# Kernel optimization log

Measured on AMD Instinct MI355X. Metric: run time of the kernel, lower is better.

Reference implementation:

```python
import jax, jax.numpy as jnp
import numpy as np

EMB_DIM = 128
MID = 192  # ceil(1.5 * emb_dim)
VOCAB = 3000
KCLS = 5
B = 16
S = 128
EPS = 1e-5


def _linear_init(k, fin, fout):
    k1, k2 = jax.random.split(k)
    bound = 1.0 / np.sqrt(fin)
    W = jax.random.uniform(k1, (fin, fout), minval=-bound, maxval=bound, dtype=jnp.float32)
    b = jax.random.uniform(k2, (fout,), minval=-bound, maxval=bound, dtype=jnp.float32)
    return W, b


def setup_inputs() -> dict:
    key = jax.random.key(0)
    ks = jax.random.split(key, 7)
    emb = jax.random.normal(ks[0], (VOCAB, EMB_DIM), dtype=jnp.float32)
    W1, b1 = _linear_init(ks[1], 2 * EMB_DIM, MID)   # encoder layer 1
    W2, b2 = _linear_init(ks[2], MID, EMB_DIM)       # encoder layer 2
    W3, b3 = _linear_init(ks[3], EMB_DIM, MID)       # decoder layer 1
    W4, b4 = _linear_init(ks[4], MID, 2 * EMB_DIM)   # decoder layer 2
    Wk, bk = _linear_init(ks[5], EMB_DIM, KCLS)      # soft head
    inputs = jax.random.randint(ks[6], (B, S), 0, VOCAB, dtype=jnp.int64)
    return dict(inputs=inputs, emb=emb, W1=W1, b1=b1, W2=W2, b2=b2,
                W3=W3, b3=b3, W4=W4, b4=b4, Wk=Wk, bk=bk)


def _forward(inputs, emb, W1, b1, W2, b2, W3, b3, W4, b4, Wk, bk):
    X = emb[inputs]                      # (B,S,m)
    Bs, Sl, m = X.shape
    bidx = jnp.arange(Bs)
    karr = jnp.arange(Sl)
    jarr = jnp.arange(Sl - 1)

    def step(carry, t):
        nodes, counts, acc = carry       # (B,S,m), (B,S), (B,)
        L = Sl - t                       # current active list length
        right, left = nodes[:, 1:], nodes[:, :-1]          # pair j = (node[j+1], node[j])
        y = (jnp.concatenate([right, left], -1) @ W1 + b1) @ W2 + b2   # (B,S-1,m)
        xx = (y @ W3 + b3) @ W4 + b4                                    # (B,S-1,2m)
        # torch cross_entropy with float-vector target: -sum(target * log_softmax(input))
        ls1 = -(right * jax.nn.log_softmax(xx[..., :m], -1)).sum(-1)
        ls2 = -(left * jax.nn.log_softmax(xx[..., m:], -1)).sum(-1)
        n1, n2 = counts[:, 1:], counts[:, :-1]
        loss = ((n1 + EPS) * ls1 + (n2 + EPS) * ls2) / (n1 + n2 + EPS)
        valid = jarr < (L - 1)                                          # only first L-1 pairs active
        idx = jnp.argmin(jnp.where(valid[None, :], loss, jnp.inf), axis=1)  # (B,)
        acc = acc + jnp.take_along_axis(loss, idx[:, None], 1)[:, 0]
        father_x = jnp.take_along_axis(y, idx[:, None, None], 1)[:, 0]  # (B,m)
        # faithful bug: lc = nodelist[idx-1] (python wrap to L-1 when idx==0), rc = nodelist[idx]
        lc_idx = jnp.where(idx == 0, L - 1, idx - 1)
        father_cnt = (jnp.take_along_axis(counts, idx[:, None], 1)[:, 0]
                      + jnp.take_along_axis(counts, lc_idx[:, None], 1)[:, 0])
        pos = jnp.maximum(idx - 1, 0)
        # new list: drop lc and rc, father lands at pos; gather map reproduces list insert/remove
        src = jnp.where((idx[:, None] == 0) | (karr[None, :] < idx[:, None] - 1),
                        karr[None, :], karr[None, :] + 1)
        src = jnp.minimum(src, Sl - 1)
        nodes = jnp.take_along_axis(nodes, src[:, :, None], 1).at[bidx, pos].set(father_x)
        counts = jnp.take_along_axis(counts, src, 1).at[bidx, pos].set(father_cnt)
        return (nodes, counts, acc), None

    init = (X, jnp.ones((Bs, Sl), X.dtype), jnp.zeros((Bs,), X.dtype))
    (nodes, counts, acc), _ = jax.lax.scan(step, init, jnp.arange(Sl - 1))
    pred = jnp.argmax(nodes[:, 0] @ Wk + bk, axis=-1)   # argmax softmax == argmax logits
    return pred, acc.sum() / Bs


def reference(inputs, emb, W1, b1, W2, b2, W3, b3, W4, b4, Wk, bk):
    return _forward(inputs, emb, W1, b1, W2, b2, W3, b3, W4, b4, Wk, bk)
```

## Files before the change

kernel.cpp:

```cpp
#include <hip/hip_runtime.h>
#include <math.h>

#define EMB 128
#define MID 192
#define SEQ 128
#define BATCH 16
#define NPAIR 127
#define KCLS 5
#define EPSF 1e-5f

#define OFF_WYT   0
#define OFF_BY    32768
#define OFF_WXXT  32896
#define OFF_BXX   65664
#define OFF_NODES 65920
#define OFF_YC    328064
#define OFF_L0    588160

__global__ void k_comp(const float* __restrict__ W1, const float* __restrict__ b1,
                       const float* __restrict__ W2, const float* __restrict__ b2,
                       const float* __restrict__ W3, const float* __restrict__ b3,
                       const float* __restrict__ W4, const float* __restrict__ b4,
                       float* __restrict__ ws) {
    int tid = blockIdx.x * blockDim.x + threadIdx.x;
    if (tid < 32768) {
        int k = tid >> 7, o = tid & 127;
        float a = 0.f;
        for (int j = 0; j < MID; ++j) a += W1[k*MID+j] * W2[j*EMB+o];
        int ch = k >> 5, jj = k & 31;
        ws[OFF_WYT + (size_t)(o*8 + ch)*32 + jj] = a;
    } else if (tid < 65536) {
        int t = tid - 32768;
        int k = t >> 8, c = t & 255;
        float a = 0.f;
        for (int j = 0; j < MID; ++j) a += W3[k*MID+j] * W4[j*256+c];
        int ch = k >> 5, jj = k & 31;
        ws[OFF_WXXT + (size_t)(c*4 + ch)*32 + jj] = a;
    } else if (tid < 65536 + 128) {
        int o = tid - 65536;
        float a = b2[o];
        for (int j = 0; j < MID; ++j) a += b1[j] * W2[j*EMB+o];
        ws[OFF_BY + o] = a;
    } else if (tid < 65536 + 128 + 256) {
        int o = tid - 65536 - 128;
        float a = b4[o];
        for (int j = 0; j < MID; ++j) a += b3[j] * W4[j*256+o];
        ws[OFF_BXX + o] = a;
    }
}

__global__ void k_nodes(const int* __restrict__ inp, const float* __restrict__ emb,
                        float* __restrict__ ws) {
    int tid = blockIdx.x * blockDim.x + threadIdx.x;
    if (tid >= BATCH*SEQ*EMB) return;
    int d = tid & 127;
    int bs = tid >> 7;
    int tok = inp[bs];
    ws[OFF_NODES + tid] = emb[tok*EMB + d];
}

#define DPPF(x, ctrl) __int_as_float(__builtin_amdgcn_update_dpp(0, __float_as_int(x), (ctrl), 0xF, 0xF, true))
#define DPPI(x, ctrl) __builtin_amdgcn_update_dpp(0, (x), (ctrl), 0xF, 0xF, true)
#define SWZ4F(x)  __int_as_float(__builtin_amdgcn_ds_swizzle(__float_as_int(x), 0x101F))
#define SWZ16F(x) __int_as_float(__builtin_amdgcn_ds_swizzle(__float_as_int(x), 0x401F))
#define SWZ16I(x) __builtin_amdgcn_ds_swizzle((x), 0x401F)

__global__ void __launch_bounds__(512, 1) k_init(float* __restrict__ ws) {
    __shared__ float s_x[2][2*EMB];
    __shared__ float s_red[4][2][EMB];
    __shared__ float s_redx[2][2][256];
    __shared__ float s_y[2][EMB];
    __shared__ float s_by[EMB];
    __shared__ float s_bxx[2*EMB];
    __shared__ float s_ls[2][2];
    int tid = threadIdx.x;
    int b = blockIdx.x >> 3, g = blockIdx.x & 7;
    int q4 = tid >> 7, o = tid & 127;
    int hh = tid >> 8, c = tid & 255;
    float wy[64], wxx[64];
    {
        const float4* gw = (const float4*)(ws + OFF_WYT);
        #pragma unroll
        for (int i = 0; i < 16; ++i) {
            float4 v = gw[((size_t)o*8 + q4*2 + (i>>3))*8 + (i&7)];
            wy[4*i]=v.x; wy[4*i+1]=v.y; wy[4*i+2]=v.z; wy[4*i+3]=v.w;
        }
        const float4* gx = (const float4*)(ws + OFF_WXXT);
        #pragma unroll
        for (int i = 0; i < 16; ++i) {
            float4 v = gx[((size_t)c*4 + hh*2 + (i>>3))*8 + (i&7)];
            wxx[4*i]=v.x; wxx[4*i+1]=v.y; wxx[4*i+2]=v.z; wxx[4*i+3]=v.w;
        }
    }
    if (tid < EMB) s_by[tid] = ws[OFF_BY + tid];
    if (tid < 2*EMB) s_bxx[tid] = ws[OFF_BXX + tid];
    const float* nodes = ws + OFF_NODES + (size_t)b*SEQ*EMB;
    float* yc = ws + OFF_YC + (size_t)b*NPAIR*EMB;
    int p_s = tid >> 8, kk = tid & 255;
    __syncthreads();
    for (int i = 0; i < 8; ++i) {
        int base = g*16 + i*2;
        {
            int j = base + p_s;
            int jj = j < NPAIR ? j : NPAIR - 1;
            s_x[p_s][kk] = nodes[(jj + (kk < 128 ? 1 : 0))*EMB + (kk & 127)];
        }
        __syncthreads();
        float a0 = 0.f, a1 = 0.f;
        #pragma unroll
        for (int j = 0; j < 64; ++j) {
            float w = wy[j];
            a0 += s_x[0][q4*64 + j] * w;
            a1 += s_x[1][q4*64 + j] * w;
        }
        s_red[q4][0][o] = a0;
        s_red[q4][1][o] = a1;
        __syncthreads();
        if (tid < 256) {
            int p = tid >> 7, oo = tid & 127;
            float yv = s_red[0][p][oo] + s_red[1][p][oo] + s_red[2][p][oo] + s_red[3][p][oo] + s_by[oo];
            s_y[p][oo] = yv;
            int j2 = base + p;
            if (j2 < NPAIR) yc[(size_t)j2*EMB + oo] = yv;
        }
        __syncthreads();
        float c0 = 0.f, c1 = 0.f;
        #pragma unroll
        for (int j = 0; j < 64; ++j) {
            float w = wxx[j];
            c0 += s_y[0][hh*64 + j] * w;
            c1 += s_y[1][hh*64 + j] * w;
        }
        s_redx[hh][0][c] = c0;
        s_redx[hh][1][c] = c1;
        __syncthreads();
        if (tid < 256) {
            int w = tid >> 6, lane = tid & 63;
            int p2 = w >> 1, h2 = w & 1;
            int cA = h2*128 + lane, cB = cA + 64;
            float v0 = s_redx[0][p2][cA] + s_redx[1][p2][cA] + s_bxx[cA];
            float v1 = s_redx[0][p2][cB] + s_redx[1][p2][cB] + s_bxx[cB];
            float m = fmaxf(v0, v1);
            for (int s = 32; s; s >>= 1) m = fmaxf(m, __shfl_xor(m, s, 64));
            float se = expf(v0 - m) + expf(v1 - m);
            for (int s = 32; s; s >>= 1) se += __shfl_xor(se, s, 64);
            float lse = m + logf(se);
            float o0 = s_x[p2][cA], o1 = s_x[p2][cB];
            float term = o0*(v0 - lse) + o1*(v1 - lse);
            for (int s = 32; s; s >>= 1) term += __shfl_xor(term, s, 64);
            if (lane == 0) s_ls[p2][h2] = -term;
        }
        __syncthreads();
        if (tid < 2) {
            int j2 = base + tid;
            if (j2 < NPAIR) {
                float l = ((1.f+EPSF)*s_ls[tid][0] + (1.f+EPSF)*s_ls[tid][1]) / (2.f + EPSF);
                ws[OFF_L0 + b*NPAIR + j2] = l;
            }
        }
        __syncthreads();
    }
}

#define SX(p, c) s_x[p][(((c) >> 6)*72) + ((c) & 63)]

__global__ void __launch_bounds__(1024, 4) __attribute__((amdgpu_waves_per_eu(4, 4)))
k_seq(float* __restrict__ ws,
      const float* __restrict__ Wk, const float* __restrict__ bkv,
      float* __restrict__ out) {
    __shared__ float s_nodes[SEQ*EMB];
    __shared__ float s_yc[NPAIR*EMB];
    __shared__ float s_x[2][4*72];
    __shared__ float s_y[2][EMB];
    __shared__ float s_xx[2][2*EMB];
    __shared__ float s_by[EMB];
    __shared__ float s_bxx[2*EMB];
    __shared__ float s_ls[2][2];
    __shared__ float s_loss[2][SEQ];
    __shared__ float s_cnt[2][SEQ];
    __shared__ int   s_nslot[2][SEQ];
    __shared__ int   s_yslot[2][SEQ];
    __shared__ float s_restv[4];
    __shared__ int   s_resti[4];
    __shared__ float s_log[KCLS];

    int tid = threadIdx.x;
    int b = blockIdx.x;
    float wy32[32], wxx32[32];
    {
        const float4* gw = (const float4*)(ws + OFF_WYT) + (size_t)tid*8;
        #pragma unroll
        for (int i = 0; i < 8; ++i) { float4 v = gw[i]; wy32[4*i]=v.x; wy32[4*i+1]=v.y; wy32[4*i+2]=v.z; wy32[4*i+3]=v.w; }
        const float4* gx = (const float4*)(ws + OFF_WXXT) + (size_t)tid*8;
        #pragma unroll
        for (int i = 0; i < 8; ++i) { float4 v = gx[i]; wxx32[4*i]=v.x; wxx32[4*i+1]=v.y; wxx32[4*i+2]=v.z; wxx32[4*i+3]=v.w; }
    }
    {
        const float4* gn = (const float4*)(ws + OFF_NODES + (size_t)b*SEQ*EMB);
        float4* sn = (float4*)s_nodes;
        for (int i = tid; i < SEQ*EMB/4; i += 1024) sn[i] = gn[i];
        const float4* gy = (const float4*)(ws + OFF_YC + (size_t)b*NPAIR*EMB);
        float4* sy = (float4*)s_yc;
        for (int i = tid; i < NPAIR*EMB/4; i += 1024) sy[i] = gy[i];
    }
    if (tid < EMB) s_by[tid] = ws[OFF_BY + tid];
    if (tid < 2*EMB) s_bxx[tid] = ws[OFF_BXX + tid];
    if (tid < NPAIR) { s_loss[0][tid] = ws[OFF_L0 + b*NPAIR + tid]; s_yslot[0][tid] = tid; }
    if (tid < SEQ)   { s_cnt[0][tid] = 1.f; s_nslot[0][tid] = tid; }

    float acc = 0.f;
    int cur = 0;
    int q0c = -1, q1c = -1;
    const int ch1 = tid & 7,  o1 = tid >> 3;
    const int ch2 = tid & 3,  c2 = tid >> 2;
    const int sp = tid >> 8, skk = tid & 255;
    __syncthreads();

    #pragma unroll 1
    for (int t = 0; t < NPAIR; ++t) {
        const int L = SEQ - t;
        if (t > 0) {
            {
                float a0 = 0.f, a1 = 0.f;
                const float* x0 = &s_x[0][(ch1 >> 1)*72 + (ch1 & 1)*32];
                const float* x1 = &s_x[1][(ch1 >> 1)*72 + (ch1 & 1)*32];
                #pragma unroll
                for (int j = 0; j < 32; ++j) { float w = wy32[j]; a0 = fmaf(x0[j], w, a0); a1 = fmaf(x1[j], w, a1); }
                a0 += DPPF(a0, 0xB1); a1 += DPPF(a1, 0xB1);
                a0 += DPPF(a0, 0x4E); a1 += DPPF(a1, 0x4E);
                a0 += SWZ4F(a0);      a1 += SWZ4F(a1);
                if (ch1 == 0) {
                    float bb = s_by[o1];
                    float y0 = a0 + bb, y1 = a1 + bb;
                    s_y[0][o1] = y0; s_y[1][o1] = y1;
                    s_yc[(size_t)s_yslot[cur][q0c]*EMB + o1] = y0;
                    s_yc[(size_t)s_yslot[cur][q1c]*EMB + o1] = y1;
                }
            }
            __syncthreads();
            {
                float c0 = 0.f, c1 = 0.f;
                const float* y0p = &s_y[0][ch2*32];
                const float* y1p = &s_y[1][ch2*32];
                #pragma unroll
                for (int j = 0; j < 32; ++j) { float w = wxx32[j]; c0 = fmaf(y0p[j], w, c0); c1 = fmaf(y1p[j], w, c1); }
                c0 += DPPF(c0, 0xB1); c1 += DPPF(c1, 0xB1);
                c0 += DPPF(c0, 0x4E); c1 += DPPF(c1, 0x4E);
                if (ch2 == 0) {
                    float bb = s_bxx[c2];
                    s_xx[0][c2] = c0 + bb;
                    s_xx[1][c2] = c1 + bb;
                }
            }
            __syncthreads();
        }
        if (t > 0 && tid < 128) {
            int p2 = tid >> 6, h2 = (tid >> 5) & 1, l5 = tid & 31;
            int base = h2*128 + l5;
            float v0 = s_xx[p2][base],      v1 = s_xx[p2][base+32];
            float v2 = s_xx[p2][base+64],   v3 = s_xx[p2][base+96];
            float o0 = SX(p2, base),        o1v = SX(p2, base+32);
            float o2 = SX(p2, base+64),     o3 = SX(p2, base+96);
            float m   = fmaxf(fmaxf(v0, v1), fmaxf(v2, v3));
            float sov = v0*o0 + v1*o1v + v2*o2 + v3*o3;
            float so  = (o0 + o1v) + (o2 + o3);
            m = fmaxf(m, DPPF(m, 0xB1));  sov += DPPF(sov, 0xB1);  so += DPPF(so, 0xB1);
            m = fmaxf(m, DPPF(m, 0x4E));  sov += DPPF(sov, 0x4E);  so += DPPF(so, 0x4E);
            m = fmaxf(m, DPPF(m, 0x124)); sov += DPPF(sov, 0x124); so += DPPF(so, 0x124);
            m = fmaxf(m, DPPF(m, 0x128)); sov += DPPF(sov, 0x128); so += DPPF(so, 0x128);
            m = fmaxf(m, SWZ16F(m));      sov += SWZ16F(sov);      so += SWZ16F(so);
            float se = expf(v0 - m) + expf(v1 - m) + expf(v2 - m) + expf(v3 - m);
            se += DPPF(se, 0xB1);
            se += DPPF(se, 0x4E);
            se += DPPF(se, 0x124);
            se += DPPF(se, 0x128);
            se += SWZ16F(se);
            if (l5 == 0) s_ls[p2][h2] = (m + logf(se))*so - sov;
        } else if (tid >= 128 && tid < 256) {
            int j = tid - 128;
            float v = (j <= L-2 && j != q0c && j != q1c) ? s_loss[cur][j] : INFINITY;
            int ii = j;
            {   float ov = DPPF(v, 0xB1);  int oi = DPPI(ii, 0xB1);
                bool tk = (ov < v) || (ov == v && oi < ii); v = tk ? ov : v; ii = tk ? oi : ii; }
            {   float ov = DPPF(v, 0x4E);  int oi = DPPI(ii, 0x4E);
                bool tk = (ov < v) || (ov == v && oi < ii); v = tk ? ov : v; ii = tk ? oi : ii; }
            {   float ov = DPPF(v, 0x124); int oi = DPPI(ii, 0x124);
                bool tk = (ov < v) || (ov == v && oi < ii); v = tk ? ov : v; ii = tk ? oi : ii; }
            {   float ov = DPPF(v, 0x128); int oi = DPPI(ii, 0x128);
                bool tk = (ov < v) || (ov == v && oi < ii); v = tk ? ov : v; ii = tk ? oi : ii; }
            {   float ov = SWZ16F(v);      int oi = SWZ16I(ii);
                bool tk = (ov < v) || (ov == v && oi < ii); v = tk ? ov : v; ii = tk ? oi : ii; }
            if ((j & 31) == 0) { s_restv[j >> 5] = v; s_resti[j >> 5] = ii; }
        }
        __syncthreads();
        float l0 = INFINITY, l1 = INFINITY;
        if (t > 0) {
            float n1a = s_cnt[cur][q0c+1], n2a = s_cnt[cur][q0c];
            l0 = ((n1a + EPSF)*s_ls[0][0] + (n2a + EPSF)*s_ls[0][1]) / (n1a + n2a + EPSF);
            float n1b = s_cnt[cur][q1c+1], n2b = s_cnt[cur][q1c];
            l1 = ((n1b + EPSF)*s_ls[1][0] + (n2b + EPSF)*s_ls[1][1]) / (n1b + n2b + EPSF);
        }
        float bv = s_restv[0]; int bi = s_resti[0];
        #pragma unroll
        for (int g = 1; g < 4; ++g) {
            float rv = s_restv[g]; int ri = s_resti[g];
            if (rv < bv || (rv == bv && ri < bi)) { bv = rv; bi = ri; }
        }
        if (t > 0) {
            if (l1 < bv || (l1 == bv && q1c < bi)) { bv = l1; bi = q1c; }
            if (l0 < bv || (l0 == bv && q0c < bi)) { bv = l0; bi = q0c; }
        }
        if (tid == 0) acc += bv;
        const int idx = bi;
        const int pos = idx > 0 ? idx - 1 : 0;
        const bool dS = idx > 0;
        const float fcnt = s_cnt[cur][idx] + s_cnt[cur][idx == 0 ? L-1 : idx-1];
        const int slotFr = s_nslot[cur][pos];
        const int ysIr   = s_yslot[cur][idx];
        const int nxt = cur ^ 1;
        if (tid < NPAIR) {
            int sh = (dS && tid >= pos+1 && tid <= L-3) ? 1 : 0;
            int sj = tid + sh;
            float v = (sj == q0c) ? l0 : (sj == q1c) ? l1 : s_loss[cur][sj];
            s_loss[nxt][tid]  = v;
            s_yslot[nxt][tid] = s_yslot[cur][sj];
        }
        if (tid < SEQ) {
            int sh = (dS && tid >= pos+1 && tid <= L-2) ? 1 : 0;
            s_cnt[nxt][tid]   = (tid == pos) ? fcnt : s_cnt[cur][tid + sh];
            s_nslot[nxt][tid] = s_nslot[cur][tid + sh];
        }
        q0c = pos >= 1 ? pos - 1 : 0;
        q1c = pos;
        if (tid < EMB) s_nodes[slotFr*EMB + tid] = s_yc[(size_t)ysIr*EMB + tid];
        if (tid < 512) {
            int qq = (sp ? q1c : q0c) + (skk < 128 ? 1 : 0);
            bool sYc = (qq == q1c);
            int sh = (dS && qq >= pos+1 && qq <= L-2) ? 1 : 0;
            int ms = s_nslot[cur][qq + sh];
            float xv = sYc ? s_yc[(size_t)ysIr*EMB + (skk & 127)]
                           : s_nodes[(size_t)ms*EMB + (skk & 127)];
            s_x[sp][((skk >> 6)*72) + (skk & 63)] = xv;
        }
        cur = nxt;
        __syncthreads();
    }
    {
        int w = tid >> 6, l = tid & 63;
        if (w < KCLS) {
            const float* root = s_nodes + (size_t)s_nslot[cur][0]*EMB;
            float p = root[2*l]*Wk[(2*l)*KCLS + w] + root[2*l+1]*Wk[(2*l+1)*KCLS + w];
            for (int s = 32; s; s >>= 1) p += __shfl_xor(p, s, 64);
            if (l == 0) s_log[w] = p + bkv[w];
        }
    }
    __syncthreads();
    if (tid == 0) {
        int best = 0;
        for (int cc = 1; cc < KCLS; ++cc) if (s_log[cc] > s_log[best]) best = cc;
        out[b] = (float)best;
        atomicAdd(&out[BATCH], acc * (1.f/16.f));
    }
}

extern "C" void kernel_launch(void* const* d_in, const int* in_sizes, int n_in,
                              void* d_out, int out_size, void* d_ws, size_t ws_size,
                              hipStream_t stream) {
    const int*   inp = (const int*)d_in[0];
    const float* emb = (const float*)d_in[1];
    const float* W1  = (const float*)d_in[2];
    const float* b1  = (const float*)d_in[3];
    const float* W2  = (const float*)d_in[4];
    const float* b2  = (const float*)d_in[5];
    const float* W3  = (const float*)d_in[6];
    const float* b3  = (const float*)d_in[7];
    const float* W4  = (const float*)d_in[8];
    const float* b4  = (const float*)d_in[9];
    const float* Wk  = (const float*)d_in[10];
    const float* bk  = (const float*)d_in[11];
    float* out = (float*)d_out;
    float* ws  = (float*)d_ws;

    hipMemsetAsync(d_out, 0, (size_t)out_size * sizeof(float), stream);

    k_comp<<<(65920 + 255) / 256, 256, 0, stream>>>(W1, b1, W2, b2, W3, b3, W4, b4, ws);
    k_nodes<<<(BATCH*SEQ*EMB + 255) / 256, 256, 0, stream>>>(inp, emb, ws);
    k_init<<<BATCH * 8, 512, 0, stream>>>(ws);
    k_seq<<<BATCH, 1024, 0, stream>>>(ws, Wk, bk, out);
}
```

Measured before the change: 524.2 us.

## Shrink sequential kernel to 256 threads with 128-register weight slices per thread

The sequential merge kernel drops from 1024 to 256 threads per block. Each thread now holds 128 weights for each of the two composed matrices in registers, pinned with empty asm so they stay there. The matvecs therefore need at most one DPP reduction step instead of three-level cross-lane reductions, and each wave handles more work. The weight layout in the precompute kernel is changed to match. The aim is to cut per-step synchronisation and reduction overhead in the latency-bound serial loop, at the cost of very high register pressure and fewer threads doing the per-step bookkeeping.

```diff
diff --git a/kernel.cpp b/kernel.cpp
--- a/kernel.cpp
+++ b/kernel.cpp
@@ -27,15 +27,13 @@
         int k = tid >> 7, o = tid & 127;
         float a = 0.f;
         for (int j = 0; j < MID; ++j) a += W1[k*MID+j] * W2[j*EMB+o];
-        int ch = k >> 5, jj = k & 31;
-        ws[OFF_WYT + (size_t)(o*8 + ch)*32 + jj] = a;
+        ws[OFF_WYT + (size_t)(o*2 + (k >> 7))*128 + (k & 127)] = a;
     } else if (tid < 65536) {
         int t = tid - 32768;
         int k = t >> 8, c = t & 255;
         float a = 0.f;
         for (int j = 0; j < MID; ++j) a += W3[k*MID+j] * W4[j*256+c];
-        int ch = k >> 5, jj = k & 31;
-        ws[OFF_WXXT + (size_t)(c*4 + ch)*32 + jj] = a;
+        ws[OFF_WXXT + (size_t)c*128 + k] = a;
     } else if (tid < 65536 + 128) {
         int o = tid - 65536;
         float a = b2[o];
@@ -61,9 +59,10 @@
 
 #define DPPF(x, ctrl) __int_as_float(__builtin_amdgcn_update_dpp(0, __float_as_int(x), (ctrl), 0xF, 0xF, true))
 #define DPPI(x, ctrl) __builtin_amdgcn_update_dpp(0, (x), (ctrl), 0xF, 0xF, true)
-#define SWZ4F(x)  __int_as_float(__builtin_amdgcn_ds_swizzle(__float_as_int(x), 0x101F))
 #define SWZ16F(x) __int_as_float(__builtin_amdgcn_ds_swizzle(__float_as_int(x), 0x401F))
 #define SWZ16I(x) __builtin_amdgcn_ds_swizzle((x), 0x401F)
+
+#define PIN128(arr) { _Pragma("unroll") for (int _i = 0; _i < 128; ++_i) asm volatile("" : "+v"(arr[_i])); }
 
 __global__ void __launch_bounds__(512, 1) k_init(float* __restrict__ ws) {
     __shared__ float s_x[2][2*EMB];
@@ -79,18 +78,12 @@
     int hh = tid >> 8, c = tid & 255;
     float wy[64], wxx[64];
     {
-        const float4* gw = (const float4*)(ws + OFF_WYT);
-        #pragma unroll
-        for (int i = 0; i < 16; ++i) {
-            float4 v = gw[((size_t)o*8 + q4*2 + (i>>3))*8 + (i&7)];
-            wy[4*i]=v.x; wy[4*i+1]=v.y; wy[4*i+2]=v.z; wy[4*i+3]=v.w;
-        }
-        const float4* gx = (const float4*)(ws + OFF_WXXT);
-        #pragma unroll
-        for (int i = 0; i < 16; ++i) {
-            float4 v = gx[((size_t)c*4 + hh*2 + (i>>3))*8 + (i&7)];
-            wxx[4*i]=v.x; wxx[4*i+1]=v.y; wxx[4*i+2]=v.z; wxx[4*i+3]=v.w;
-        }
+        const float4* gw = (const float4*)(ws + OFF_WYT) + ((size_t)(o*2 + (q4 >> 1))*32 + (q4 & 1)*16);
+        #pragma unroll
+        for (int i = 0; i < 16; ++i) { float4 v = gw[i]; wy[4*i]=v.x; wy[4*i+1]=v.y; wy[4*i+2]=v.z; wy[4*i+3]=v.w; }
+        const float4* gx = (const float4*)(ws + OFF_WXXT) + ((size_t)c*32 + hh*16);
+        #pragma unroll
+        for (int i = 0; i < 16; ++i) { float4 v = gx[i]; wxx[4*i]=v.x; wxx[4*i+1]=v.y; wxx[4*i+2]=v.z; wxx[4*i+3]=v.w; }
     }
     if (tid < EMB) s_by[tid] = ws[OFF_BY + tid];
     if (tid < 2*EMB) s_bxx[tid] = ws[OFF_BXX + tid];
@@ -164,7 +157,7 @@
 
 #define SX(p, c) s_x[p][(((c) >> 6)*72) + ((c) & 63)]
 
-__global__ void __launch_bounds__(1024, 4) __attribute__((amdgpu_waves_per_eu(4, 4)))
+__global__ void __launch_bounds__(256) __attribute__((amdgpu_waves_per_eu(1, 1)))
 k_seq(float* __restrict__ ws,
       const float* __restrict__ Wk, const float* __restrict__ bkv,
       float* __restrict__ out) {
@@ -186,22 +179,23 @@
 
     int tid = threadIdx.x;
     int b = blockIdx.x;
-    float wy32[32], wxx32[32];
+    float wy[128], wxx[128];
     {
-        const float4* gw = (const float4*)(ws + OFF_WYT) + (size_t)tid*8;
-        #pragma unroll
-        for (int i = 0; i < 8; ++i) { float4 v = gw[i]; wy32[4*i]=v.x; wy32[4*i+1]=v.y; wy32[4*i+2]=v.z; wy32[4*i+3]=v.w; }
-        const float4* gx = (const float4*)(ws + OFF_WXXT) + (size_t)tid*8;
-        #pragma unroll
-        for (int i = 0; i < 8; ++i) { float4 v = gx[i]; wxx32[4*i]=v.x; wxx32[4*i+1]=v.y; wxx32[4*i+2]=v.z; wxx32[4*i+3]=v.w; }
-    }
+        const float4* gw = (const float4*)(ws + OFF_WYT) + (size_t)tid*32;
+        #pragma unroll
+        for (int i = 0; i < 32; ++i) { float4 v = gw[i]; wy[4*i]=v.x; wy[4*i+1]=v.y; wy[4*i+2]=v.z; wy[4*i+3]=v.w; }
+        const float4* gx = (const float4*)(ws + OFF_WXXT) + (size_t)tid*32;
+        #pragma unroll
+        for (int i = 0; i < 32; ++i) { float4 v = gx[i]; wxx[4*i]=v.x; wxx[4*i+1]=v.y; wxx[4*i+2]=v.z; wxx[4*i+3]=v.w; }
+    }
+    PIN128(wy); PIN128(wxx);
     {
         const float4* gn = (const float4*)(ws + OFF_NODES + (size_t)b*SEQ*EMB);
         float4* sn = (float4*)s_nodes;
-        for (int i = tid; i < SEQ*EMB/4; i += 1024) sn[i] = gn[i];
+        for (int i = tid; i < SEQ*EMB/4; i += 256) sn[i] = gn[i];
         const float4* gy = (const float4*)(ws + OFF_YC + (size_t)b*NPAIR*EMB);
         float4* sy = (float4*)s_yc;
-        for (int i = tid; i < NPAIR*EMB/4; i += 1024) sy[i] = gy[i];
+        for (int i = tid; i < NPAIR*EMB/4; i += 256) sy[i] = gy[i];
     }
     if (tid < EMB) s_by[tid] = ws[OFF_BY + tid];
     if (tid < 2*EMB) s_bxx[tid] = ws[OFF_BXX + tid];
@@ -211,9 +205,7 @@
     float acc = 0.f;
     int cur = 0;
     int q0c = -1, q1c = -1;
-    const int ch1 = tid & 7,  o1 = tid >> 3;
-    const int ch2 = tid & 3,  c2 = tid >> 2;
-    const int sp = tid >> 8, skk = tid & 255;
+    const int ch1 = tid & 1, o1 = tid >> 1;
     __syncthreads();
 
     #pragma unroll 1
@@ -221,14 +213,20 @@
         const int L = SEQ - t;
         if (t > 0) {
             {
-                float a0 = 0.f, a1 = 0.f;
-                const float* x0 = &s_x[0][(ch1 >> 1)*72 + (ch1 & 1)*32];
-                const float* x1 = &s_x[1][(ch1 >> 1)*72 + (ch1 & 1)*32];
+                float a0 = 0.f, a1 = 0.f, b0 = 0.f, b1 = 0.f;
+                const float* x0a = &s_x[0][(2*ch1)*72];
+                const float* x0b = &s_x[0][(2*ch1+1)*72];
+                const float* x1a = &s_x[1][(2*ch1)*72];
+                const float* x1b = &s_x[1][(2*ch1+1)*72];
                 #pragma unroll
-                for (int j = 0; j < 32; ++j) { float w = wy32[j]; a0 = fmaf(x0[j], w, a0); a1 = fmaf(x1[j], w, a1); }
+                for (int j = 0; j < 64; ++j) {
+                    a0 = fmaf(x0a[j], wy[j], a0);
+                    a1 = fmaf(x1a[j], wy[j], a1);
+                    b0 = fmaf(x0b[j], wy[64+j], b0);
+                    b1 = fmaf(x1b[j], wy[64+j], b1);
+                }
+                a0 += b0; a1 += b1;
                 a0 += DPPF(a0, 0xB1); a1 += DPPF(a1, 0xB1);
-                a0 += DPPF(a0, 0x4E); a1 += DPPF(a1, 0x4E);
-                a0 += SWZ4F(a0);      a1 += SWZ4F(a1);
                 if (ch1 == 0) {
                     float bb = s_by[o1];
                     float y0 = a0 + bb, y1 = a1 + bb;
@@ -239,18 +237,19 @@
             }
             __syncthreads();
             {
-                float c0 = 0.f, c1 = 0.f;
-                const float* y0p = &s_y[0][ch2*32];
-                const float* y1p = &s_y[1][ch2*32];
+                float c0 = 0.f, c1 = 0.f, d0 = 0.f, d1 = 0.f;
+                const float* y0p = s_y[0];
+                const float* y1p = s_y[1];
                 #pragma unroll
-                for (int j = 0; j < 32; ++j) { float w = wxx32[j]; c0 = fmaf(y0p[j], w, c0); c1 = fmaf(y1p[j], w, c1); }
-                c0 += DPPF(c0, 0xB1); c1 += DPPF(c1, 0xB1);
-                c0 += DPPF(c0, 0x4E); c1 += DPPF(c1, 0x4E);
-                if (ch2 == 0) {
-                    float bb = s_bxx[c2];
-                    s_xx[0][c2] = c0 + bb;
-                    s_xx[1][c2] = c1 + bb;
+                for (int j = 0; j < 64; ++j) {
+                    c0 = fmaf(y0p[j],    wxx[j],    c0);
+                    c1 = fmaf(y1p[j],    wxx[j],    c1);
+                    d0 = fmaf(y0p[64+j], wxx[64+j], d0);
+                    d1 = fmaf(y1p[64+j], wxx[64+j], d1);
                 }
+                float bb = s_bxx[tid];
+                s_xx[0][tid] = c0 + d0 + bb;
+                s_xx[1][tid] = c1 + d1 + bb;
             }
             __syncthreads();
         }
@@ -333,7 +332,10 @@
         q0c = pos >= 1 ? pos - 1 : 0;
         q1c = pos;
         if (tid < EMB) s_nodes[slotFr*EMB + tid] = s_yc[(size_t)ysIr*EMB + tid];
-        if (tid < 512) {
+        #pragma unroll
+        for (int rep = 0; rep < 2; ++rep) {
+            int gi = tid + rep*256;
+            int sp = gi >> 8, skk = gi & 255;
             int qq = (sp ? q1c : q0c) + (skk < 128 ? 1 : 0);
             bool sYc = (qq == q1c);
             int sh = (dS && qq >= pos+1 && qq <= L-2) ? 1 : 0;
@@ -346,8 +348,8 @@
         __syncthreads();
     }
     {
-        int w = tid >> 6, l = tid & 63;
-        if (w < KCLS) {
+        int l = tid & 63;
+        for (int w = tid >> 6; w < KCLS; w += 4) {
             const float* root = s_nodes + (size_t)s_nslot[cur][0]*EMB;
             float p = root[2*l]*Wk[(2*l)*KCLS + w] + root[2*l+1]*Wk[(2*l+1)*KCLS + w];
             for (int s = 32; s; s >>= 1) p += __shfl_xor(p, s, 64);
@@ -386,5 +388,5 @@
     k_comp<<<(65920 + 255) / 256, 256, 0, stream>>>(W1, b1, W2, b2, W3, b3, W4, b4, ws);
     k_nodes<<<(BATCH*SEQ*EMB + 255) / 256, 256, 0, stream>>>(inp, emb, ws);
     k_init<<<BATCH * 8, 512, 0, stream>>>(ws);
-    k_seq<<<BATCH, 1024, 0, stream>>>(ws, Wk, bk, out);
-}
+    k_seq<<<BATCH, 256, 0, stream>>>(ws, Wk, bk, out);
+}
```

Result: slower. 620.6 us (+18.4%).
